# Kernel tuning notes

Measured on AMD Instinct MI355X. Metric: run time of the kernel, lower is better.

## Reference

```python
import jax, jax.numpy as jnp
import numpy as np

C = 32          # backbone_channels[-4]
RATIO = 0.05    # keep_topk ratio

def conv2d(x, w, b, pad, groups=1):
    y = jax.lax.conv_general_dilated(x, w, (1, 1), [(pad, pad), (pad, pad)],
                                     dimension_numbers=('NCHW', 'OIHW', 'NCHW'),
                                     feature_group_count=groups)
    return y + b[None, :, None, None]

def bn(x, g, b, m, v, eps=1e-5):
    return (x - m[None, :, None, None]) * jax.lax.rsqrt(v[None, :, None, None] + eps) \
           * g[None, :, None, None] + b[None, :, None, None]

def up2x_bilinear(x):
    B, Ch, H, W = x.shape
    return jax.image.resize(x, (B, Ch, 2 * H, 2 * W), method='bilinear')

def setup_inputs() -> dict:
    key = jax.random.key(0)
    ks = jax.random.split(key, 20)
    f32 = jnp.float32
    d = {
        'feats4x': jax.random.normal(ks[0], (16, C, 128, 128), f32),
        'feats2x': jax.random.normal(ks[1], (16, 16, 256, 256), f32),
        'classify_logits': jax.random.normal(ks[2], (16, 1, 256, 256), f32),
        # SparseConvNeXtBlock params
        'dw_w': jax.random.normal(ks[3], (C, 1, 7, 7), f32) * 0.05,
        'dw_b': jnp.zeros((C,), f32),
        'ln_g': jnp.ones((C,), f32), 'ln_b': jnp.zeros((C,), f32),
        'pw1_w': jax.random.normal(ks[4], (C, C), f32) * 0.05, 'pw1_b': jnp.zeros((C,), f32),
        'grn_g': jnp.ones((C,), f32) * 0.1, 'grn_b': jnp.zeros((C,), f32),
        'pw2_w': jax.random.normal(ks[5], (C, C), f32) * 0.05, 'pw2_b': jnp.zeros((C,), f32),
        'up_w': jax.random.normal(ks[6], (8, C, 3, 3), f32) * 0.05, 'up_b': jnp.zeros((8,), f32),
        'bn1_g': jnp.ones((8,), f32), 'bn1_b': jnp.zeros((8,), f32),
        'bn1_m': jnp.zeros((8,), f32), 'bn1_v': jnp.ones((8,), f32),
        'sh_w': jax.random.normal(ks[7], (8, 16, 3, 3), f32) * 0.05, 'sh_b': jnp.zeros((8,), f32),
        'bn2_g': jnp.ones((8,), f32), 'bn2_b': jnp.zeros((8,), f32),
        'bn2_m': jnp.zeros((8,), f32), 'bn2_v': jnp.ones((8,), f32),
        'last_w': jax.random.normal(ks[8], (4, 16, 3, 3), f32) * 0.05, 'last_b': jnp.zeros((4,), f32),
        'last2_w': jax.random.normal(ks[9], (1, 4, 5, 5), f32) * 0.05, 'last2_b': jnp.zeros((1,), f32),
    }
    return d

def _forward(feats4x, feats2x, classify_logits,
             dw_w, dw_b, ln_g, ln_b, pw1_w, pw1_b, grn_g, grn_b, pw2_w, pw2_b,
             up_w, up_b, bn1_g, bn1_b, bn1_m, bn1_v,
             sh_w, sh_b, bn2_g, bn2_b, bn2_m, bn2_v,
             last_w, last_b, last2_w, last2_b):
    prob = jax.nn.sigmoid(classify_logits[:, :, ::2, ::2])  # [B,1,H4,W4]
    B, _, H, W = prob.shape
    k = int(RATIO * H * W)
    flat = prob.reshape(B, -1)
    vals, _ = jax.lax.top_k(flat, k)
    thr = vals[:, -1]
    mask = (flat > thr[:, None]).reshape(B, 1, H, W).astype(feats4x.dtype)

    # --- SparseConvNeXtBlock (mlp_ratio=1, linear_pw_conv, GRN, layer_scale=0) ---
    shortcut = feats4x
    x = conv2d(feats4x, dw_w, dw_b, 3, groups=C) * mask     # sparse dwconv 7x7
    xh = x.transpose(0, 2, 3, 1)                            # NHWC
    mu = xh.mean(-1, keepdims=True)
    var = ((xh - mu) ** 2).mean(-1, keepdims=True)
    xh = (xh - mu) * jax.lax.rsqrt(var + 1e-6) * ln_g + ln_b
    xh = xh * mask.transpose(0, 2, 3, 1)                    # sparse LN2d
    xh = xh @ pw1_w.T + pw1_b
    xh = jax.nn.gelu(xh, approximate=False)
    gx = jnp.sqrt(jnp.sum(xh ** 2, axis=(1, 2), keepdims=True))  # GRN, [B,1,1,C]
    nx = gx / (jnp.mean(gx, axis=-1, keepdims=True) + 1e-6)
    xh = grn_g * (xh * nx) + grn_b + xh
    xh = xh @ pw2_w.T + pw2_b
    x = shortcut + xh.transpose(0, 3, 1, 2)

    # --- upsample module (part of sparse_head list) ---
    x = up2x_bilinear(bn(conv2d(x, up_w, up_b, 1), bn1_g, bn1_b, bn1_m, bn1_v))  # [B,8,H2,W2]
    s = jax.nn.relu(bn(conv2d(feats2x, sh_w, sh_b, 1), bn2_g, bn2_b, bn2_m, bn2_v))
    out = jnp.concatenate([x, s], axis=1)                   # [B,16,H2,W2]
    out = up2x_bilinear(conv2d(out, last_w, last_b, 1))     # [B,4,H,W]
    out = conv2d(out, last2_w, last2_b, 2)                  # [B,1,H,W]
    return jax.nn.sigmoid(out), jax.nn.sigmoid(classify_logits)

def reference(feats4x, feats2x, classify_logits,
              dw_w, dw_b, ln_g, ln_b, pw1_w, pw1_b, grn_g, grn_b, pw2_w, pw2_b,
              up_w, up_b, bn1_g, bn1_b, bn1_m, bn1_v,
              sh_w, sh_b, bn2_g, bn2_b, bn2_m, bn2_v,
              last_w, last_b, last2_w, last2_b):
    return _forward(feats4x, feats2x, classify_logits,
                    dw_w, dw_b, ln_g, ln_b, pw1_w, pw1_b, grn_g, grn_b, pw2_w, pw2_b,
                    up_w, up_b, bn1_g, bn1_b, bn1_m, bn1_v,
                    sh_w, sh_b, bn2_g, bn2_b, bn2_m, bn2_v,
                    last_w, last_b, last2_w, last2_b)
```

## Files before the change

### kernel.cpp

```cpp
#include <hip/hip_runtime.h>
#include <math.h>


#define NSLOT 824

typedef __attribute__((ext_vector_type(4))) float f32x4;

struct __attribute__((packed, aligned(4))) f4u { float a0, a1, a2, a3; };

__device__ __forceinline__ void nt_store4(float* p, float a, float b, float c,
                                          float d) {
  f32x4 v = {a, b, c, d};
  __builtin_nontemporal_store(v, reinterpret_cast<f32x4*>(p));
}

__device__ __forceinline__ float erf_fast(float x) {
  float ax = fabsf(x);
  float t = __builtin_amdgcn_rcpf(fmaf(0.3275911f, ax, 1.f));
  float poly = t * fmaf(t, fmaf(t, fmaf(t, fmaf(t, 1.061405429f, -1.453152027f),
                                        1.421413741f), -0.284496736f), 0.254829592f);
  float r = 1.f - poly * __expf(-ax * ax);
  return copysignf(r, x);
}

__global__ void k_sig(const float* __restrict__ lg, float* __restrict__ out) {
  int i = blockIdx.x * 256 + threadIdx.x;
  float4 v = reinterpret_cast<const float4*>(lg)[i];
  nt_store4(out + (i << 2), 1.f / (1.f + __expf(-v.x)), 1.f / (1.f + __expf(-v.y)),
            1.f / (1.f + __expf(-v.z)), 1.f / (1.f + __expf(-v.w)));
}

__global__ __launch_bounds__(1024) void k_topk(const float* __restrict__ lg,
                                               int* __restrict__ actIdx,
                                               int* __restrict__ n_act) {
  __shared__ unsigned keys[16384];
  __shared__ unsigned hist[256];
  __shared__ unsigned sh_prefix, sh_krem;
  __shared__ int sh_cnt;
  int b = blockIdx.x, t = threadIdx.x;
  if (t < 256) hist[t] = 0u;
  if (t == 0) { sh_prefix = 0u; sh_krem = 819u; sh_cnt = 0; }
  __syncthreads();
  for (int i = t; i < 16384; i += 1024) {
    float vF = lg[(b << 16) + ((i >> 7) << 9) + ((i & 127) << 1)];
    unsigned u = __float_as_uint(vF);
    unsigned key = (u & 0x80000000u) ? ~u : (u | 0x80000000u);
    keys[i] = key;
    atomicAdd(&hist[key >> 24], 1u);
  }
  for (int pass = 0; pass < 4; ++pass) {
    __syncthreads();
    if (t == 0) {
      unsigned krem = sh_krem, c = 0;
      int bin = 255;
      for (; bin >= 0; --bin) {
        unsigned c2 = c + hist[bin];
        if (c2 >= krem) break;
        c = c2;
      }
      sh_prefix = (sh_prefix << 8) | (unsigned)bin;
      sh_krem = krem - c;
    }
    __syncthreads();
    if (pass < 3) {
      if (t < 256) hist[t] = 0u;
      __syncthreads();
      int shift = 16 - 8 * pass;
      unsigned pref = sh_prefix;
      for (int i = t; i < 16384; i += 1024) {
        unsigned key = keys[i];
        if ((key >> (shift + 8)) == pref) atomicAdd(&hist[(key >> shift) & 255u], 1u);
      }
    }
  }
  __syncthreads();
  unsigned thrkey = sh_prefix;
  for (int i = t; i < 16384; i += 1024) {
    if (keys[i] > thrkey) {
      int s = atomicAdd(&sh_cnt, 1);
      actIdx[b * NSLOT + s] = i;
    }
  }
  __syncthreads();
  if (t == 0) n_act[b] = sh_cnt;
}

__global__ __launch_bounds__(256, 4) void k_dws(
    const float* __restrict__ f4, const int* __restrict__ actIdx,
    const int* __restrict__ n_act, const float* __restrict__ dw_w,
    const float* __restrict__ dw_b, const float* __restrict__ lng,
    const float* __restrict__ lnb, const float* __restrict__ w1,
    const float* __restrict__ b1, float* __restrict__ y1c,
    float* __restrict__ gss) {
  int b = blockIdx.y;
  int slot0 = blockIdx.x << 3;
  int na = n_act[b];
  if (slot0 >= na) return;
  int t = threadIdx.x;
  __shared__ float wdwT[49][32];
  __shared__ float w1sT[32][32];
  __shared__ float xhs[8][32];
  __shared__ float pacc[8][32];
  __shared__ float sLng[32], sLnb[32], sB1[32], sDwB[32];
  for (int i = t; i < 1568; i += 256) wdwT[i % 49][i / 49] = dw_w[i];
  for (int i = t; i < 1024; i += 256) w1sT[i & 31][i >> 5] = w1[i];
  if (t < 32) { sLng[t] = lng[t]; sLnb[t] = lnb[t]; sB1[t] = b1[t]; sDwB[t] = dw_b[t]; }
  __syncthreads();
  int px = t >> 5, c = t & 31;
  int slot = slot0 + px;
  bool valid = slot < na;
  int pos = valid ? actIdx[b * NSLOT + slot] : -1;
  float xv = 0.f;
  if (valid) {
    int y = pos >> 7, x = pos & 127;
    const float* base = f4 + (((b << 5) + c) << 14);
    float a = sDwB[c];
    bool inner = (x >= 3) && (x <= 123);
#pragma unroll
    for (int dy = -3; dy <= 3; ++dy) {
      int yy = y + dy;
      if ((unsigned)yy < 128u) {
        const float* rp = base + (yy << 7) + x;
        if (inner) {
          f4u A4 = *reinterpret_cast<const f4u*>(rp - 3);
          f4u B4 = *reinterpret_cast<const f4u*>(rp + 1);
          float r[7] = {A4.a0, A4.a1, A4.a2, A4.a3, B4.a0, B4.a1, B4.a2};
#pragma unroll
          for (int k = 0; k < 7; ++k)
            a = fmaf(r[k], wdwT[(dy + 3) * 7 + k][c], a);
        } else {
#pragma unroll
          for (int k = 0; k < 7; ++k) {
            int xx = x - 3 + k;
            if ((unsigned)xx < 128u)
              a = fmaf(rp[k - 3], wdwT[(dy + 3) * 7 + k][c], a);
          }
        }
      }
    }
    xv = a;
  }
  float s1 = xv, s2 = xv * xv;
#pragma unroll
  for (int m = 1; m < 32; m <<= 1) {
    s1 += __shfl_xor(s1, m, 64);
    s2 += __shfl_xor(s2, m, 64);
  }
  float mu = s1 * 0.03125f;
  float var = fmaxf(s2 * 0.03125f - mu * mu, 0.f);
  float rs = rsqrtf(var + 1e-6f);
  float xh = (xv - mu) * rs * sLng[c] + sLnb[c];
  xhs[px][c] = valid ? xh : 0.f;
  __syncthreads();
  int j = c;
  float a = sB1[j];
#pragma unroll
  for (int cc = 0; cc < 32; ++cc) a = fmaf(xhs[px][cc], w1sT[cc][j], a);
  float gl = 0.5f * a * (1.f + erf_fast(a * 0.70710678f));
  pacc[px][j] = valid ? gl * gl : 0.f;
  if (valid) y1c[(b * NSLOT + slot) * 32 + j] = gl;
  __syncthreads();
  if (t < 32) {
    float s = 0.f;
#pragma unroll
    for (int q = 0; q < 8; ++q) s += pacc[q][t];
    atomicAdd(&gss[(b << 5) + t], s);
  }
}

__global__ void k_grn(const float* __restrict__ gss, const int* __restrict__ n_act,
                      const float* __restrict__ grng, const float* __restrict__ grnb,
                      const float* __restrict__ w2, const float* __restrict__ b2,
                      const float* __restrict__ b1, float* __restrict__ w2sT,
                      float* __restrict__ bias2, float* __restrict__ Kconst) {
  int b = blockIdx.x, t = threadIdx.x;
  __shared__ float gxs[32], sc[32], gb1[32];
  if (t < 32) {
    float u = b1[t];
    float gl = 0.5f * u * (1.f + erf_fast(u * 0.70710678f));
    gb1[t] = gl;
    float cnt = (float)(16384 - n_act[b]);
    gxs[t] = sqrtf(gss[(b << 5) + t] + cnt * gl * gl);
  }
  __syncthreads();
  if (t < 32) {
    float m = 0.f;
#pragma unroll
    for (int c = 0; c < 32; ++c) m += gxs[c];
    m = m * 0.03125f + 1e-6f;
    sc[t] = grng[t] * (gxs[t] / m) + 1.f;
  }
  __syncthreads();
  for (int i = t; i < 1024; i += 256) {
    int c = i >> 5, j = i & 31;
    w2sT[(b << 10) + i] = w2[j * 32 + c] * sc[c];
  }
  if (t < 32) {
    float s = 0.f;
#pragma unroll
    for (int c = 0; c < 32; ++c) s += grnb[c] * w2[t * 32 + c];
    float bb = s + b2[t];
    bias2[(b << 5) + t] = bb;
    float k = bb;
#pragma unroll
    for (int c = 0; c < 32; ++c) k = fmaf(gb1[c] * sc[c], w2[t * 32 + c], k);
    Kconst[(b << 5) + t] = k;
  }
}

__global__ __launch_bounds__(256, 4) void k_pw2d(
    const float* __restrict__ Kc, const float* __restrict__ f4,
    float* __restrict__ xo) {
  int b = blockIdx.x >> 6, chunk = blockIdx.x & 63, t = threadIdx.x;
  int p = t & 63, j0 = (t >> 6) << 3;
  int ty = chunk >> 3, tx = chunk & 7;
  int y = (ty << 4) + (p >> 2), xb = (tx << 4) + ((p << 2) & 15);
  float K[8];
#pragma unroll
  for (int j = 0; j < 8; ++j) K[j] = Kc[(b << 5) + j0 + j];
  float acc[4][8];
#pragma unroll
  for (int j = 0; j < 8; ++j) {
    float4 s4 = *reinterpret_cast<const float4*>(
        f4 + (((b << 5) + j0 + j) << 14) + (y << 7) + xb);
    acc[0][j] = s4.x + K[j]; acc[1][j] = s4.y + K[j];
    acc[2][j] = s4.z + K[j]; acc[3][j] = s4.w + K[j];
  }
#pragma unroll
  for (int i = 0; i < 4; ++i) {
    float* op = xo + (((b << 14) + (y << 7) + xb + i) << 5) + j0;
    *reinterpret_cast<float4*>(op) = make_float4(acc[i][0], acc[i][1], acc[i][2], acc[i][3]);
    *reinterpret_cast<float4*>(op + 4) = make_float4(acc[i][4], acc[i][5], acc[i][6], acc[i][7]);
  }
}

__global__ __launch_bounds__(256, 4) void k_pw2s(
    const float* __restrict__ y1c, const int* __restrict__ actIdx,
    const int* __restrict__ n_act, const float* __restrict__ w2sT,
    const float* __restrict__ bias2, const float* __restrict__ f4,
    float* __restrict__ xo) {
  int b = blockIdx.y;
  int slot0 = blockIdx.x << 3;
  int na = n_act[b];
  if (slot0 >= na) return;
  int t = threadIdx.x;
  __shared__ float w2s[32][32];
  __shared__ float ys[8][32];
  __shared__ float sb2[32];
  for (int i = t; i < 1024; i += 256) w2s[i >> 5][i & 31] = w2sT[(b << 10) + i];
  if (t < 32) sb2[t] = bias2[(b << 5) + t];
  int px = t >> 5, j = t & 31;
  int slot = slot0 + px;
  bool valid = slot < na;
  ys[px][j] = valid ? y1c[(b * NSLOT + slot) * 32 + j] : 0.f;
  __syncthreads();
  if (valid) {
    int pos = actIdx[b * NSLOT + slot];
    float a = sb2[j];
#pragma unroll
    for (int cc = 0; cc < 32; ++cc) a = fmaf(ys[px][cc], w2s[cc][j], a);
    a += f4[(((b << 5) + j) << 14) + pos];
    xo[(((b << 14) + pos) << 5) + j] = a;
  }
}

template <int IC, int OC, int HH, int WW, int MODE>
__global__ __launch_bounds__(256, 3) void k_conv3(
    const float* __restrict__ xin,
    const float* __restrict__ wgt, const float* __restrict__ bias,
    const float* __restrict__ bng, const float* __restrict__ bnb,
    const float* __restrict__ bnm, const float* __restrict__ bnv,
    float* __restrict__ out) {
  constexpr int NG = IC / 4;
  int bx = blockIdx.x << 5, by = blockIdx.y << 5, b = blockIdx.z;
  int t = threadIdx.x;
  int py = t >> 3, px0 = (t & 7) << 2;
  __shared__ __align__(16) float4 xt[34 * 35];
  __shared__ __align__(16) float4 wt[NG * 9 * OC];
  for (int idx = t; idx < NG * 9 * OC; idx += 256) {
    int g = idx / (9 * OC);
    int rem = idx - g * 9 * OC;
    int tap = rem / OC, o = rem - tap * OC;
    int ky = tap / 3, kx = tap - ky * 3;
    float4 wv;
    wv.x = wgt[((o * IC + g * 4 + 0) * 3 + ky) * 3 + kx];
    wv.y = wgt[((o * IC + g * 4 + 1) * 3 + ky) * 3 + kx];
    wv.z = wgt[((o * IC + g * 4 + 2) * 3 + ky) * 3 + kx];
    wv.w = wgt[((o * IC + g * 4 + 3) * 3 + ky) * 3 + kx];
    wt[idx] = wv;
  }
  float acc[4][OC];
#pragma unroll
  for (int i = 0; i < 4; ++i)
#pragma unroll
    for (int o = 0; o < OC; ++o) acc[i][o] = 0.f;

  float4 sr[5];
  auto loadg = [&](int g) {
#pragma unroll
    for (int k = 0; k < 5; ++k) {
      int i = t + (k << 8);
      float4 v = make_float4(0.f, 0.f, 0.f, 0.f);
      if (i < 1156) {
        int r = i / 34, c = i - r * 34;
        int gy = by - 1 + r, gx = bx - 1 + c;
        if ((unsigned)gy < (unsigned)HH && (unsigned)gx < (unsigned)WW) {
          if (MODE == 1) {
            const float* p0 = xin + (((b * IC + (g << 2)) * HH + gy) * WW) + gx;
            v.x = p0[0]; v.y = p0[HH * WW]; v.z = p0[2 * HH * WW]; v.w = p0[3 * HH * WW];
          } else {
            v = *reinterpret_cast<const float4*>(
                xin + (((b * HH) + gy) * WW + gx) * IC + (g << 2));
          }
        }
      }
      sr[k] = v;
    }
  };
  auto writeg = [&]() {
#pragma unroll
    for (int k = 0; k < 5; ++k) {
      int i = t + (k << 8);
      if (i < 1156) {
        int r = i / 34;
        xt[r * 35 + (i - r * 34)] = sr[k];
      }
    }
  };

  loadg(0);
#pragma unroll 1
  for (int g = 0; g < NG; ++g) {
    writeg();
    __syncthreads();
    if (g + 1 < NG) loadg(g + 1);
#pragma unroll
    for (int ky = 0; ky < 3; ++ky) {
      float4 xr[6];
#pragma unroll
      for (int q = 0; q < 6; ++q) xr[q] = xt[(py + ky) * 35 + px0 + q];
#pragma unroll
      for (int kx = 0; kx < 3; ++kx)
#pragma unroll
        for (int o = 0; o < OC; ++o) {
          float4 wv = wt[(g * 9 + ky * 3 + kx) * OC + o];
#pragma unroll
          for (int i = 0; i < 4; ++i) {
            float4 xv = xr[kx + i];
            acc[i][o] = fmaf(xv.w, wv.w, fmaf(xv.z, wv.z, fmaf(xv.y, wv.y, fmaf(xv.x, wv.x, acc[i][o]))));
          }
        }
    }
    __syncthreads();
  }
  float scl[OC], sbs[OC];
#pragma unroll
  for (int o = 0; o < OC; ++o) {
    float rs = rsqrtf(bnv[o] + 1e-5f) * bng[o];
    scl[o] = rs;
    sbs[o] = (bias[o] - bnm[o]) * rs + bnb[o];
  }
  int gy = by + py;
#pragma unroll
  for (int i = 0; i < 4; ++i) {
    int gx = bx + px0 + i;
    float ov[OC];
#pragma unroll
    for (int o = 0; o < OC; ++o) {
      float u = acc[i][o] * scl[o] + sbs[o];
      if (MODE == 1) u = fmaxf(u, 0.f);
      ov[o] = u;
    }
    float* op = out + ((b * HH * WW) + gy * WW + gx) * OC;
    *reinterpret_cast<float4*>(op) = make_float4(ov[0], ov[1], ov[2], ov[3]);
    if (OC == 8)
      *reinterpret_cast<float4*>(op + 4) = make_float4(ov[4], ov[5], ov[6], ov[7]);
  }
}

__global__ __launch_bounds__(256, 3) void k_lastup(
    const float* __restrict__ E, const float* __restrict__ D,
    const float* __restrict__ wgt, const float* __restrict__ bias,
    float* __restrict__ out) {
  int bx = blockIdx.x << 5, by = blockIdx.y << 5, b = blockIdx.z;
  int t = threadIdx.x;
  int py = t >> 3, px0 = (t & 7) << 2;
  __shared__ __align__(16) float4 et[19][22][2];
  __shared__ __align__(16) float4 xt[34 * 35];
  __shared__ __align__(16) float4 wt[144];
  for (int idx = t; idx < 144; idx += 256) {
    int g = idx / 36, rem = idx - g * 36;
    int tap = rem >> 2, o = rem & 3;
    int ky = tap / 3, kx = tap - ky * 3;
    float4 wv;
    wv.x = wgt[((o * 16 + g * 4 + 0) * 3 + ky) * 3 + kx];
    wv.y = wgt[((o * 16 + g * 4 + 1) * 3 + ky) * 3 + kx];
    wv.z = wgt[((o * 16 + g * 4 + 2) * 3 + ky) * 3 + kx];
    wv.w = wgt[((o * 16 + g * 4 + 3) * 3 + ky) * 3 + kx];
    wt[idx] = wv;
  }
  float acc[4][4];
#pragma unroll
  for (int i = 0; i < 4; ++i)
#pragma unroll
    for (int o = 0; o < 4; ++o) acc[i][o] = 0.f;

  float4 dreg[5];
  auto loadD = [&](int h) {
#pragma unroll
    for (int k = 0; k < 5; ++k) {
      int i = t + (k << 8);
      float4 v = make_float4(0.f, 0.f, 0.f, 0.f);
      if (i < 1156) {
        int r = i / 34, c = i - r * 34;
        int gy = by - 1 + r, gx = bx - 1 + c;
        if ((unsigned)gy < 256u && (unsigned)gx < 256u)
          v = *reinterpret_cast<const float4*>(
              D + (((b << 16) + (gy << 8) + gx) << 3) + (h << 2));
      }
      dreg[k] = v;
    }
  };
  auto compute = [&](int g) {
#pragma unroll
    for (int ky = 0; ky < 3; ++ky) {
      float4 xr[6];
#pragma unroll
      for (int q = 0; q < 6; ++q) xr[q] = xt[(py + ky) * 35 + px0 + q];
#pragma unroll
      for (int kx = 0; kx < 3; ++kx)
#pragma unroll
        for (int o = 0; o < 4; ++o) {
          float4 wv = wt[(g * 9 + ky * 3 + kx) * 4 + o];
#pragma unroll
          for (int i = 0; i < 4; ++i) {
            float4 xv = xr[kx + i];
            acc[i][o] = fmaf(xv.w, wv.w, fmaf(xv.z, wv.z, fmaf(xv.y, wv.y, fmaf(xv.x, wv.x, acc[i][o]))));
          }
        }
    }
  };

  loadD(0);
  int ey0 = (by >> 1) - 1, ex0 = (bx >> 1) - 3;
#pragma unroll
  for (int k = 0; k < 4; ++k) {
    int i = t + (k << 8);
    if (i < 836) {
      int h = i & 1, q = i >> 1;
      int r = q / 22, c = q - r * 22;
      int er = min(max(ey0 + r, 0), 127), ec = min(max(ex0 + c, 0), 127);
      et[r][c][h] = *reinterpret_cast<const float4*>(
          E + (((b << 14) + (er << 7) + ec) << 3) + (h << 2));
    }
  }
#pragma unroll 1
  for (int h = 0; h < 2; ++h) {
    __syncthreads();
#pragma unroll
    for (int k = 0; k < 5; ++k) {
      int i = t + (k << 8);
      if (i < 1156) {
        int r = i / 34;
        xt[r * 35 + (i - r * 34)] = dreg[k];
      }
    }
    __syncthreads();
    if (h == 0) loadD(1);
    compute(2 + h);
  }
#pragma unroll 1
  for (int h = 0; h < 2; ++h) {
    __syncthreads();
#pragma unroll
    for (int k = 0; k < 5; ++k) {
      int i = t + (k << 8);
      if (i < 1156) {
        int r = i / 34, c = i - r * 34;
        int gy = by - 1 + r, gx = bx - 1 + c;
        float4 uv = make_float4(0.f, 0.f, 0.f, 0.f);
        if ((unsigned)gy < 256u && (unsigned)gx < 256u) {
          int r0 = (gy - 1) >> 1, c0 = (gx - 1) >> 1;
          float fy = (gy & 1) ? 0.25f : 0.75f;
          float fx = (gx & 1) ? 0.25f : 0.75f;
          int ra = max(r0, 0) - ey0, rb = min(r0 + 1, 127) - ey0;
          int ca = max(c0, 0) - ex0, cb = min(c0 + 1, 127) - ex0;
          float w00 = (1.f - fy) * (1.f - fx), w01 = (1.f - fy) * fx;
          float w10 = fy * (1.f - fx), w11 = fy * fx;
          float4 a = et[ra][ca][h], bq = et[ra][cb][h];
          float4 cq = et[rb][ca][h], dq = et[rb][cb][h];
          uv.x = w00 * a.x + w01 * bq.x + w10 * cq.x + w11 * dq.x;
          uv.y = w00 * a.y + w01 * bq.y + w10 * cq.y + w11 * dq.y;
          uv.z = w00 * a.z + w01 * bq.z + w10 * cq.z + w11 * dq.z;
          uv.w = w00 * a.w + w01 * bq.w + w10 * cq.w + w11 * dq.w;
        }
        xt[r * 35 + c] = uv;
      }
    }
    __syncthreads();
    compute(h);
  }
  float b0 = bias[0], b1v = bias[1], b2v = bias[2], b3v = bias[3];
  int gy = by + py;
#pragma unroll
  for (int i = 0; i < 4; ++i) {
    int gx = bx + px0 + i;
    float* op = out + (((b << 16) + (gy << 8) + gx) << 2);
    *reinterpret_cast<float4*>(op) = make_float4(acc[i][0] + b0, acc[i][1] + b1v,
                                                 acc[i][2] + b2v, acc[i][3] + b3v);
  }
}

__global__ __launch_bounds__(256, 3) void k_final(
    const float* __restrict__ v4, const float* __restrict__ w5,
    const float* __restrict__ b5, float* __restrict__ out) {
  int bx = blockIdx.x << 5, by = blockIdx.y << 5, b = blockIdx.z;
  int t = threadIdx.x;
  __shared__ __align__(16) float4 vt[20 * 21];
  __shared__ __align__(16) float4 ut[36 * 37];
  __shared__ __align__(16) float4 w5s[25];
  if (t < 25) {
    w5s[t] = make_float4(w5[t], w5[25 + t], w5[50 + t], w5[75 + t]);
  }
  int vy0 = (by >> 1) - 2, vx0 = (bx >> 1) - 2;
  for (int i = t; i < 400; i += 256) {
    int r = i / 20, c = i - r * 20;
    int gy = vy0 + r, gx = vx0 + c;
    float4 v = make_float4(0.f, 0.f, 0.f, 0.f);
    if (gy >= 0 && gy < 256 && gx >= 0 && gx < 256)
      v = *reinterpret_cast<const float4*>(v4 + ((b << 16) + gy * 256 + gx) * 4);
    vt[r * 21 + c] = v;
  }
  __syncthreads();
  for (int i = t; i < 36 * 36; i += 256) {
    int r = i / 36, c = i - r * 36;
    int yy = by - 2 + r, xx = bx - 2 + c;
    float4 uv = make_float4(0.f, 0.f, 0.f, 0.f);
    if (yy >= 0 && yy < 512 && xx >= 0 && xx < 512) {
      int r0 = (yy - 1) >> 1, c0 = (xx - 1) >> 1;
      float fy = (yy & 1) ? 0.25f : 0.75f;
      float fx = (xx & 1) ? 0.25f : 0.75f;
      int ra = max(r0, 0) - vy0, rb = min(r0 + 1, 255) - vy0;
      int ca = max(c0, 0) - vx0, cb = min(c0 + 1, 255) - vx0;
      float4 a = vt[ra * 21 + ca], bq = vt[ra * 21 + cb];
      float4 cq = vt[rb * 21 + ca], dq = vt[rb * 21 + cb];
      float w00 = (1.f - fy) * (1.f - fx), w01 = (1.f - fy) * fx;
      float w10 = fy * (1.f - fx), w11 = fy * fx;
      uv.x = w00 * a.x + w01 * bq.x + w10 * cq.x + w11 * dq.x;
      uv.y = w00 * a.y + w01 * bq.y + w10 * cq.y + w11 * dq.y;
      uv.z = w00 * a.z + w01 * bq.z + w10 * cq.z + w11 * dq.z;
      uv.w = w00 * a.w + w01 * bq.w + w10 * cq.w + w11 * dq.w;
    }
    ut[r * 37 + c] = uv;
  }
  __syncthreads();
  float bb = b5[0];
  int py = t >> 3, px0 = (t & 7) << 2;
  float a0 = bb, a1 = bb, a2 = bb, a3 = bb;
#pragma unroll
  for (int ky = 0; ky < 5; ++ky) {
    float4 xr[8];
#pragma unroll
    for (int q = 0; q < 8; ++q) xr[q] = ut[(py + ky) * 37 + px0 + q];
#pragma unroll
    for (int kx = 0; kx < 5; ++kx) {
      float4 w = w5s[ky * 5 + kx];
      float4 x0 = xr[kx], x1 = xr[kx + 1], x2 = xr[kx + 2], x3 = xr[kx + 3];
      a0 = fmaf(x0.w, w.w, fmaf(x0.z, w.z, fmaf(x0.y, w.y, fmaf(x0.x, w.x, a0))));
      a1 = fmaf(x1.w, w.w, fmaf(x1.z, w.z, fmaf(x1.y, w.y, fmaf(x1.x, w.x, a1))));
      a2 = fmaf(x2.w, w.w, fmaf(x2.z, w.z, fmaf(x2.y, w.y, fmaf(x2.x, w.x, a2))));
      a3 = fmaf(x3.w, w.w, fmaf(x3.z, w.z, fmaf(x3.y, w.y, fmaf(x3.x, w.x, a3))));
    }
  }
  int oy = by + py, ox = bx + px0;
  nt_store4(out + (b << 18) + oy * 512 + ox,
            1.f / (1.f + __expf(-a0)), 1.f / (1.f + __expf(-a1)),
            1.f / (1.f + __expf(-a2)), 1.f / (1.f + __expf(-a3)));
}

extern "C" void kernel_launch(void* const* d_in, const int* in_sizes, int n_in,
                              void* d_out, int out_size, void* d_ws, size_t ws_size,
                              hipStream_t stream) {
  (void)in_sizes; (void)n_in; (void)out_size; (void)ws_size;
  const float* feats4x = (const float*)d_in[0];
  const float* feats2x = (const float*)d_in[1];
  const float* clg     = (const float*)d_in[2];
  const float* dw_w    = (const float*)d_in[3];
  const float* dw_b    = (const float*)d_in[4];
  const float* ln_g    = (const float*)d_in[5];
  const float* ln_b    = (const float*)d_in[6];
  const float* pw1_w   = (const float*)d_in[7];
  const float* pw1_b   = (const float*)d_in[8];
  const float* grn_g   = (const float*)d_in[9];
  const float* grn_b   = (const float*)d_in[10];
  const float* pw2_w   = (const float*)d_in[11];
  const float* pw2_b   = (const float*)d_in[12];
  const float* up_w    = (const float*)d_in[13];
  const float* up_b    = (const float*)d_in[14];
  const float* bn1_g   = (const float*)d_in[15];
  const float* bn1_b   = (const float*)d_in[16];
  const float* bn1_m   = (const float*)d_in[17];
  const float* bn1_v   = (const float*)d_in[18];
  const float* sh_w    = (const float*)d_in[19];
  const float* sh_b    = (const float*)d_in[20];
  const float* bn2_g   = (const float*)d_in[21];
  const float* bn2_b   = (const float*)d_in[22];
  const float* bn2_m   = (const float*)d_in[23];
  const float* bn2_v   = (const float*)d_in[24];
  const float* last_w  = (const float*)d_in[25];
  const float* last_b  = (const float*)d_in[26];
  const float* last2_w = (const float*)d_in[27];
  const float* last2_b = (const float*)d_in[28];
  float* outp = (float*)d_out;
  float* ws = (float*)d_ws;
  float* A     = ws;
  float* y1c   = ws + 8388608;
  int*   actIdx = (int*)(ws + 8810496);
  int*   n_act  = (int*)(ws + 8823680);
  float* D     = ws + 16777216;
  float* E     = ws + 25165824;
  float* gss   = ws + 27262976;
  float* w2sT  = gss + 512;
  float* bias2 = w2sT + 16384;
  float* Kconst = bias2 + 512;

  hipMemsetAsync(gss, 0, 512 * sizeof(float), stream);
  k_sig<<<1024, 256, 0, stream>>>(clg, outp + 4194304);
  k_topk<<<16, 1024, 0, stream>>>(clg, actIdx, n_act);
  k_dws<<<dim3(103, 16), 256, 0, stream>>>(feats4x, actIdx, n_act, dw_w, dw_b,
                                           ln_g, ln_b, pw1_w, pw1_b, y1c, gss);
  k_grn<<<16, 256, 0, stream>>>(gss, n_act, grn_g, grn_b, pw2_w, pw2_b, pw1_b,
                                w2sT, bias2, Kconst);
  k_pw2d<<<1024, 256, 0, stream>>>(Kconst, feats4x, A);
  k_pw2s<<<dim3(103, 16), 256, 0, stream>>>(y1c, actIdx, n_act, w2sT, bias2,
                                            feats4x, A);
  k_conv3<32, 8, 128, 128, 0><<<dim3(4, 4, 16), 256, 0, stream>>>(
      A, up_w, up_b, bn1_g, bn1_b, bn1_m, bn1_v, E);
  k_conv3<16, 8, 256, 256, 1><<<dim3(8, 8, 16), 256, 0, stream>>>(
      feats2x, sh_w, sh_b, bn2_g, bn2_b, bn2_m, bn2_v, D);
  k_lastup<<<dim3(8, 8, 16), 256, 0, stream>>>(E, D, last_w, last_b, A);
  k_final<<<dim3(16, 16, 16), 256, 0, stream>>>(A, last2_w, last2_b, outp);
}
```

Before: 270.7 us.

## Fuse dense residual into upsample conv via slot map; vectorize shut2x conv loads

Removes the k_pw2d pass that wrote the full dense 32-channel NHWC intermediate. k_pw2s now writes only the active-pixel results into a compact buffer. A new k_upconv builds a per-tile slot map and reads either the compact active values or feats4x plus the constant directly from NCHW. It also uses smaller 16x16 tiles, giving more blocks. The shut2x conv is specialized and loads rows as float4 vectors with a scattered shared-memory transpose. This cuts a large write/read round trip at the cost of strided per-channel loads and per-block index scans.

Result: faster. 264.6 us (-2.2%).

```diff
diff --git a/kernel.cpp b/kernel.cpp
--- a/kernel.cpp
+++ b/kernel.cpp
@@ -208,37 +208,11 @@
   }
 }
 
-__global__ __launch_bounds__(256, 4) void k_pw2d(
-    const float* __restrict__ Kc, const float* __restrict__ f4,
-    float* __restrict__ xo) {
-  int b = blockIdx.x >> 6, chunk = blockIdx.x & 63, t = threadIdx.x;
-  int p = t & 63, j0 = (t >> 6) << 3;
-  int ty = chunk >> 3, tx = chunk & 7;
-  int y = (ty << 4) + (p >> 2), xb = (tx << 4) + ((p << 2) & 15);
-  float K[8];
-#pragma unroll
-  for (int j = 0; j < 8; ++j) K[j] = Kc[(b << 5) + j0 + j];
-  float acc[4][8];
-#pragma unroll
-  for (int j = 0; j < 8; ++j) {
-    float4 s4 = *reinterpret_cast<const float4*>(
-        f4 + (((b << 5) + j0 + j) << 14) + (y << 7) + xb);
-    acc[0][j] = s4.x + K[j]; acc[1][j] = s4.y + K[j];
-    acc[2][j] = s4.z + K[j]; acc[3][j] = s4.w + K[j];
-  }
-#pragma unroll
-  for (int i = 0; i < 4; ++i) {
-    float* op = xo + (((b << 14) + (y << 7) + xb + i) << 5) + j0;
-    *reinterpret_cast<float4*>(op) = make_float4(acc[i][0], acc[i][1], acc[i][2], acc[i][3]);
-    *reinterpret_cast<float4*>(op + 4) = make_float4(acc[i][4], acc[i][5], acc[i][6], acc[i][7]);
-  }
-}
-
 __global__ __launch_bounds__(256, 4) void k_pw2s(
     const float* __restrict__ y1c, const int* __restrict__ actIdx,
     const int* __restrict__ n_act, const float* __restrict__ w2sT,
     const float* __restrict__ bias2, const float* __restrict__ f4,
-    float* __restrict__ xo) {
+    float* __restrict__ xact) {
   int b = blockIdx.y;
   int slot0 = blockIdx.x << 3;
   int na = n_act[b];
@@ -260,80 +234,189 @@
 #pragma unroll
     for (int cc = 0; cc < 32; ++cc) a = fmaf(ys[px][cc], w2s[cc][j], a);
     a += f4[(((b << 5) + j) << 14) + pos];
-    xo[(((b << 14) + pos) << 5) + j] = a;
-  }
-}
-
-template <int IC, int OC, int HH, int WW, int MODE>
-__global__ __launch_bounds__(256, 3) void k_conv3(
+    xact[(b * NSLOT + slot) * 32 + j] = a;
+  }
+}
+
+__global__ __launch_bounds__(256, 3) void k_upconv(
+    const float* __restrict__ f4, const float* __restrict__ Kc,
+    const float* __restrict__ xact, const int* __restrict__ actIdx,
+    const int* __restrict__ n_act, const float* __restrict__ wgt,
+    const float* __restrict__ bias, const float* __restrict__ bng,
+    const float* __restrict__ bnb, const float* __restrict__ bnm,
+    const float* __restrict__ bnv, float* __restrict__ out) {
+  int bx = blockIdx.x << 4, by = blockIdx.y << 4, b = blockIdx.z;
+  int t = threadIdx.x;
+  __shared__ __align__(16) float4 xt[18 * 19];
+  __shared__ __align__(16) float4 wt[576];
+  __shared__ unsigned short slotmap[324];
+  __shared__ float sKc[32];
+  for (int idx = t; idx < 576; idx += 256) {
+    int g = idx / 72, rem = idx - g * 72;
+    int tap = rem >> 3, o = rem & 7;
+    int ky = tap / 3, kx = tap - ky * 3;
+    float4 wv;
+    wv.x = wgt[((o * 32 + g * 4 + 0) * 3 + ky) * 3 + kx];
+    wv.y = wgt[((o * 32 + g * 4 + 1) * 3 + ky) * 3 + kx];
+    wv.z = wgt[((o * 32 + g * 4 + 2) * 3 + ky) * 3 + kx];
+    wv.w = wgt[((o * 32 + g * 4 + 3) * 3 + ky) * 3 + kx];
+    wt[idx] = wv;
+  }
+  if (t < 32) sKc[t] = Kc[(b << 5) + t];
+  for (int i = t; i < 324; i += 256) slotmap[i] = 0xFFFFu;
+  __syncthreads();
+  int na = n_act[b];
+  for (int i = t; i < na; i += 256) {
+    int pos = actIdx[b * NSLOT + i];
+    int y = pos >> 7, x = pos & 127;
+    unsigned r = (unsigned)(y - by + 1), c = (unsigned)(x - bx + 1);
+    if (r < 18u && c < 18u) slotmap[r * 18 + c] = (unsigned short)i;
+  }
+  __syncthreads();
+  int py = t >> 4, px = t & 15;
+  float acc[8];
+#pragma unroll
+  for (int o = 0; o < 8; ++o) acc[o] = 0.f;
+  float4 sr[2];
+  auto loadg = [&](int g) {
+#pragma unroll
+    for (int k = 0; k < 2; ++k) {
+      int i = t + (k << 8);
+      float4 v = make_float4(0.f, 0.f, 0.f, 0.f);
+      if (i < 324) {
+        int r = i / 18, c = i - r * 18;
+        int gy = by - 1 + r, gx = bx - 1 + c;
+        if ((unsigned)gy < 128u && (unsigned)gx < 128u) {
+          unsigned short s = slotmap[r * 18 + c];
+          if (s != 0xFFFFu) {
+            v = *reinterpret_cast<const float4*>(
+                xact + ((b * NSLOT + (int)s) << 5) + (g << 2));
+          } else {
+            const float* p0 = f4 + (((b << 5) + (g << 2)) << 14) + (gy << 7) + gx;
+            v.x = p0[0] + sKc[(g << 2) + 0];
+            v.y = p0[16384] + sKc[(g << 2) + 1];
+            v.z = p0[32768] + sKc[(g << 2) + 2];
+            v.w = p0[49152] + sKc[(g << 2) + 3];
+          }
+        }
+      }
+      sr[k] = v;
+    }
+  };
+  auto writeg = [&]() {
+#pragma unroll
+    for (int k = 0; k < 2; ++k) {
+      int i = t + (k << 8);
+      if (i < 324) {
+        int r = i / 18;
+        xt[r * 19 + (i - r * 18)] = sr[k];
+      }
+    }
+  };
+  loadg(0);
+#pragma unroll 1
+  for (int g = 0; g < 8; ++g) {
+    writeg();
+    __syncthreads();
+    if (g < 7) loadg(g + 1);
+#pragma unroll
+    for (int ky = 0; ky < 3; ++ky) {
+      float4 xr[3];
+#pragma unroll
+      for (int q = 0; q < 3; ++q) xr[q] = xt[(py + ky) * 19 + px + q];
+#pragma unroll
+      for (int kx = 0; kx < 3; ++kx)
+#pragma unroll
+        for (int o = 0; o < 8; ++o) {
+          float4 wv = wt[(g * 9 + ky * 3 + kx) * 8 + o];
+          float4 xv = xr[kx];
+          acc[o] = fmaf(xv.w, wv.w, fmaf(xv.z, wv.z, fmaf(xv.y, wv.y, fmaf(xv.x, wv.x, acc[o]))));
+        }
+    }
+    __syncthreads();
+  }
+  int gy = by + py, gx = bx + px;
+  float ov[8];
+#pragma unroll
+  for (int o = 0; o < 8; ++o) {
+    float rs = rsqrtf(bnv[o] + 1e-5f) * bng[o];
+    ov[o] = acc[o] * rs + (bias[o] - bnm[o]) * rs + bnb[o];
+  }
+  float* op = out + (((b << 14) + (gy << 7) + gx) << 3);
+  *reinterpret_cast<float4*>(op) = make_float4(ov[0], ov[1], ov[2], ov[3]);
+  *reinterpret_cast<float4*>(op + 4) = make_float4(ov[4], ov[5], ov[6], ov[7]);
+}
+
+__global__ __launch_bounds__(256, 3) void k_conv3s(
     const float* __restrict__ xin,
     const float* __restrict__ wgt, const float* __restrict__ bias,
     const float* __restrict__ bng, const float* __restrict__ bnb,
     const float* __restrict__ bnm, const float* __restrict__ bnv,
     float* __restrict__ out) {
-  constexpr int NG = IC / 4;
   int bx = blockIdx.x << 5, by = blockIdx.y << 5, b = blockIdx.z;
   int t = threadIdx.x;
   int py = t >> 3, px0 = (t & 7) << 2;
   __shared__ __align__(16) float4 xt[34 * 35];
-  __shared__ __align__(16) float4 wt[NG * 9 * OC];
-  for (int idx = t; idx < NG * 9 * OC; idx += 256) {
-    int g = idx / (9 * OC);
-    int rem = idx - g * 9 * OC;
-    int tap = rem / OC, o = rem - tap * OC;
+  __shared__ __align__(16) float4 wt[4 * 9 * 8];
+  for (int idx = t; idx < 288; idx += 256) {
+    int g = idx / 72, rem = idx - g * 72;
+    int tap = rem >> 3, o = rem & 7;
     int ky = tap / 3, kx = tap - ky * 3;
     float4 wv;
-    wv.x = wgt[((o * IC + g * 4 + 0) * 3 + ky) * 3 + kx];
-    wv.y = wgt[((o * IC + g * 4 + 1) * 3 + ky) * 3 + kx];
-    wv.z = wgt[((o * IC + g * 4 + 2) * 3 + ky) * 3 + kx];
-    wv.w = wgt[((o * IC + g * 4 + 3) * 3 + ky) * 3 + kx];
+    wv.x = wgt[((o * 16 + g * 4 + 0) * 3 + ky) * 3 + kx];
+    wv.y = wgt[((o * 16 + g * 4 + 1) * 3 + ky) * 3 + kx];
+    wv.z = wgt[((o * 16 + g * 4 + 2) * 3 + ky) * 3 + kx];
+    wv.w = wgt[((o * 16 + g * 4 + 3) * 3 + ky) * 3 + kx];
     wt[idx] = wv;
   }
-  float acc[4][OC];
+  float acc[4][8];
 #pragma unroll
   for (int i = 0; i < 4; ++i)
 #pragma unroll
-    for (int o = 0; o < OC; ++o) acc[i][o] = 0.f;
-
-  float4 sr[5];
+    for (int o = 0; o < 8; ++o) acc[i][o] = 0.f;
+
+  float4 sq[6];
   auto loadg = [&](int g) {
 #pragma unroll
-    for (int k = 0; k < 5; ++k) {
+    for (int k = 0; k < 6; ++k) {
       int i = t + (k << 8);
       float4 v = make_float4(0.f, 0.f, 0.f, 0.f);
-      if (i < 1156) {
-        int r = i / 34, c = i - r * 34;
-        int gy = by - 1 + r, gx = bx - 1 + c;
-        if ((unsigned)gy < (unsigned)HH && (unsigned)gx < (unsigned)WW) {
-          if (MODE == 1) {
-            const float* p0 = xin + (((b * IC + (g << 2)) * HH + gy) * WW) + gx;
-            v.x = p0[0]; v.y = p0[HH * WW]; v.z = p0[2 * HH * WW]; v.w = p0[3 * HH * WW];
-          } else {
-            v = *reinterpret_cast<const float4*>(
-                xin + (((b * HH) + gy) * WW + gx) * IC + (g << 2));
-          }
-        }
-      }
-      sr[k] = v;
+      if (i < 1360) {
+        int cl = i / 340, rem = i - cl * 340;
+        int r = rem / 10, q = rem - r * 10;
+        int gy = by - 1 + r, gx0 = bx - 4 + (q << 2);
+        if ((unsigned)gy < 256u && (unsigned)gx0 <= 252u)
+          v = *reinterpret_cast<const float4*>(
+              xin + (((b * 16 + (g << 2) + cl) << 8) + gy) * 256 + gx0);
+      }
+      sq[k] = v;
     }
   };
   auto writeg = [&]() {
 #pragma unroll
-    for (int k = 0; k < 5; ++k) {
+    for (int k = 0; k < 6; ++k) {
       int i = t + (k << 8);
-      if (i < 1156) {
-        int r = i / 34;
-        xt[r * 35 + (i - r * 34)] = sr[k];
+      if (i < 1360) {
+        int cl = i / 340, rem = i - cl * 340;
+        int r = rem / 10, q = rem - r * 10;
+        float* bp = reinterpret_cast<float*>(&xt[r * 35]) + cl;
+        int c0 = (q << 2) - 3;
+        float vv[4] = {sq[k].x, sq[k].y, sq[k].z, sq[k].w};
+#pragma unroll
+        for (int kk = 0; kk < 4; ++kk) {
+          int c = c0 + kk;
+          if ((unsigned)c < 34u) bp[c << 2] = vv[kk];
+        }
       }
     }
   };
 
   loadg(0);
 #pragma unroll 1
-  for (int g = 0; g < NG; ++g) {
+  for (int g = 0; g < 4; ++g) {
     writeg();
     __syncthreads();
-    if (g + 1 < NG) loadg(g + 1);
+    if (g < 3) loadg(g + 1);
 #pragma unroll
     for (int ky = 0; ky < 3; ++ky) {
       float4 xr[6];
@@ -342,8 +425,8 @@
 #pragma unroll
       for (int kx = 0; kx < 3; ++kx)
 #pragma unroll
-        for (int o = 0; o < OC; ++o) {
-          float4 wv = wt[(g * 9 + ky * 3 + kx) * OC + o];
+        for (int o = 0; o < 8; ++o) {
+          float4 wv = wt[(g * 9 + ky * 3 + kx) * 8 + o];
 #pragma unroll
           for (int i = 0; i < 4; ++i) {
             float4 xv = xr[kx + i];
@@ -353,9 +436,9 @@
     }
     __syncthreads();
   }
-  float scl[OC], sbs[OC];
-#pragma unroll
-  for (int o = 0; o < OC; ++o) {
+  float scl[8], sbs[8];
+#pragma unroll
+  for (int o = 0; o < 8; ++o) {
     float rs = rsqrtf(bnv[o] + 1e-5f) * bng[o];
     scl[o] = rs;
     sbs[o] = (bias[o] - bnm[o]) * rs + bnb[o];
@@ -364,17 +447,13 @@
 #pragma unroll
   for (int i = 0; i < 4; ++i) {
     int gx = bx + px0 + i;
-    float ov[OC];
-#pragma unroll
-    for (int o = 0; o < OC; ++o) {
-      float u = acc[i][o] * scl[o] + sbs[o];
-      if (MODE == 1) u = fmaxf(u, 0.f);
-      ov[o] = u;
-    }
-    float* op = out + ((b * HH * WW) + gy * WW + gx) * OC;
+    float ov[8];
+#pragma unroll
+    for (int o = 0; o < 8; ++o)
+      ov[o] = fmaxf(acc[i][o] * scl[o] + sbs[o], 0.f);
+    float* op = out + (((b << 16) + (gy << 8) + gx) << 3);
     *reinterpret_cast<float4*>(op) = make_float4(ov[0], ov[1], ov[2], ov[3]);
-    if (OC == 8)
-      *reinterpret_cast<float4*>(op + 4) = make_float4(ov[4], ov[5], ov[6], ov[7]);
+    *reinterpret_cast<float4*>(op + 4) = make_float4(ov[4], ov[5], ov[6], ov[7]);
   }
 }
 
@@ -613,15 +692,16 @@
   const float* last2_b = (const float*)d_in[28];
   float* outp = (float*)d_out;
   float* ws = (float*)d_ws;
-  float* A     = ws;
-  float* y1c   = ws + 8388608;
-  int*   actIdx = (int*)(ws + 8810496);
-  int*   n_act  = (int*)(ws + 8823680);
-  float* D     = ws + 16777216;
-  float* E     = ws + 25165824;
-  float* gss   = ws + 27262976;
-  float* w2sT  = gss + 512;
-  float* bias2 = w2sT + 16384;
+  float* A      = ws;
+  float* y1c    = ws + 8388608;
+  float* xact   = ws + 8810496;
+  int*   actIdx = (int*)(ws + 9232384);
+  int*   n_act  = (int*)(ws + 9245568);
+  float* D      = ws + 16777216;
+  float* E      = ws + 25165824;
+  float* gss    = ws + 27262976;
+  float* w2sT   = gss + 512;
+  float* bias2  = w2sT + 16384;
   float* Kconst = bias2 + 512;
 
   hipMemsetAsync(gss, 0, 512 * sizeof(float), stream);
@@ -631,13 +711,13 @@
                                            ln_g, ln_b, pw1_w, pw1_b, y1c, gss);
   k_grn<<<16, 256, 0, stream>>>(gss, n_act, grn_g, grn_b, pw2_w, pw2_b, pw1_b,
                                 w2sT, bias2, Kconst);
-  k_pw2d<<<1024, 256, 0, stream>>>(Kconst, feats4x, A);
   k_pw2s<<<dim3(103, 16), 256, 0, stream>>>(y1c, actIdx, n_act, w2sT, bias2,
-                                            feats4x, A);
-  k_conv3<32, 8, 128, 128, 0><<<dim3(4, 4, 16), 256, 0, stream>>>(
-      A, up_w, up_b, bn1_g, bn1_b, bn1_m, bn1_v, E);
-  k_conv3<16, 8, 256, 256, 1><<<dim3(8, 8, 16), 256, 0, stream>>>(
-      feats2x, sh_w, sh_b, bn2_g, bn2_b, bn2_m, bn2_v, D);
+                                            feats4x, xact);
+  k_upconv<<<dim3(8, 8, 16), 256, 0, stream>>>(feats4x, Kconst, xact, actIdx,
+                                               n_act, up_w, up_b, bn1_g, bn1_b,
+                                               bn1_m, bn1_v, E);
+  k_conv3s<<<dim3(8, 8, 16), 256, 0, stream>>>(feats2x, sh_w, sh_b, bn2_g,
+                                               bn2_b, bn2_m, bn2_v, D);
   k_lastup<<<dim3(8, 8, 16), 256, 0, stream>>>(E, D, last_w, last_b, A);
   k_final<<<dim3(16, 16, 16), 256, 0, stream>>>(A, last2_w, last2_b, outp);
 }
```
